# Optimization experiments

Measured on AMD Instinct MI355X. Metric: run time of the kernel, lower is better.

## Reference

```python
import jax, jax.numpy as jnp
import numpy as np

NUM_HEADS = 16
D_MODEL = 1024
D_QKV = 64


def _xavier(key, shape):
    # xavier normal over last two dims (fan_in = D_MODEL, fan_out = D_QKV)
    std = float(np.sqrt(2.0 / (shape[-2] + shape[-1])))
    return jax.random.normal(key, shape, dtype=jnp.float32) * std


def setup_inputs() -> dict:
    key = jax.random.key(0)
    ks = jax.random.split(key, 9)
    B, L = 4, 2048
    q = jax.random.normal(ks[0], (B, L, D_MODEL), dtype=jnp.float32)
    k = jax.random.normal(ks[1], (B, L, D_MODEL), dtype=jnp.float32)
    v = jax.random.normal(ks[2], (B, L, D_MODEL), dtype=jnp.float32)
    mask = jax.random.randint(ks[3], (B, L, L), 0, 2, dtype=jnp.int32)
    Wq = _xavier(ks[4], (NUM_HEADS, D_MODEL, D_QKV))
    Wk = _xavier(ks[5], (NUM_HEADS, D_MODEL, D_QKV))
    Wv = _xavier(ks[6], (NUM_HEADS, D_MODEL, D_QKV))
    lim = float(1.0 / np.sqrt(D_MODEL))
    Wo_w = jax.random.uniform(ks[7], (D_MODEL, D_MODEL), minval=-lim, maxval=lim, dtype=jnp.float32)
    Wo_b = jax.random.uniform(ks[8], (D_MODEL,), minval=-lim, maxval=lim, dtype=jnp.float32)
    return {"q": q, "k": k, "v": v, "mask": mask,
            "Wq": Wq, "Wk": Wk, "Wv": Wv, "Wo_w": Wo_w, "Wo_b": Wo_b}


def reference(q, k, v, mask, Wq, Wk, Wv, Wo_w, Wo_b):
    B, L, _ = q.shape
    query = jnp.einsum('blm,nmd->bnld', q, Wq)   # [B,H,L,Dq]
    key_ = jnp.einsum('blm,nmd->bnld', k, Wk)
    value = jnp.einsum('blm,nmd->bnld', v, Wv)
    scores = jnp.einsum('bnld,bnmd->bnlm', query, key_) / jnp.sqrt(
        jnp.asarray(D_QKV, dtype=query.dtype))          # [B,H,L,L]
    scores = jnp.where(mask[:, None, :, :] == 0, jnp.asarray(-1e9, scores.dtype), scores)
    attn = jax.nn.softmax(scores, axis=-1)
    out = jnp.einsum('bnlm,bnmd->bnld', attn, value)     # [B,H,L,Dq]
    out = out.transpose(0, 2, 1, 3).reshape(B, L, D_MODEL)
    return out @ Wo_w.T + Wo_b
```

## Files before the change

kernel.cpp:

```cpp
#include <hip/hip_runtime.h>
#include <stdint.h>

typedef __bf16 bf16;
typedef __bf16 bf16x8 __attribute__((ext_vector_type(8)));
typedef float  f32x4  __attribute__((ext_vector_type(4)));
typedef uint32_t u32;
typedef uint64_t u64;

#define SCALE_L2E 0.18033688011112042f

__device__ __forceinline__ void gld_lds16(const void* gsrc, void* ldst) {
  __builtin_amdgcn_global_load_lds(
      (const __attribute__((address_space(1))) void*)gsrc,
      (__attribute__((address_space(3))) void*)ldst, 16, 0, 0);
}


__global__ void cvt_f32_bf16(const float* __restrict__ in, bf16* __restrict__ out, int n8) {
  int stride = gridDim.x * blockDim.x;
  for (int i = blockIdx.x * blockDim.x + threadIdx.x; i < n8; i += stride) {
    const float4* p = (const float4*)(in + (size_t)i * 8);
    float4 a = p[0], b = p[1];
    bf16x8 v;
    v[0]=(bf16)a.x; v[1]=(bf16)a.y; v[2]=(bf16)a.z; v[3]=(bf16)a.w;
    v[4]=(bf16)b.x; v[5]=(bf16)b.y; v[6]=(bf16)b.z; v[7]=(bf16)b.w;
    *(bf16x8*)(out + (size_t)i * 8) = v;
  }
}

__global__ void pack_w(const float* __restrict__ Wq, const float* __restrict__ Wk,
                       const float* __restrict__ Wv, const float* __restrict__ Wo,
                       bf16* __restrict__ Wt) {
  int s = blockIdx.z;
  int tid = blockIdx.x * blockDim.x + threadIdx.x;
  int n = tid >> 7, kb = tid & 127;
  const float* W = (s == 0) ? Wq : (s == 1) ? Wk : (s == 2) ? Wv : Wo;
  bf16x8 v;
  if (s < 3) {
#pragma unroll
    for (int j = 0; j < 8; ++j)
      v[j] = (bf16)W[((n >> 6) << 16) + (kb * 8 + j) * 64 + (n & 63)];
  } else {
    const float4* p = (const float4*)&W[n * 1024 + kb * 8];
    float4 a = p[0], b = p[1];
    v[0]=(bf16)a.x; v[1]=(bf16)a.y; v[2]=(bf16)a.z; v[3]=(bf16)a.w;
    v[4]=(bf16)b.x; v[5]=(bf16)b.y; v[6]=(bf16)b.z; v[7]=(bf16)b.w;
  }
  *(bf16x8*)&Wt[(size_t)s * 1048576 + (size_t)n * 1024 + kb * 8] = v;
}

__global__ void pack_mask(const int* __restrict__ mask, u32* __restrict__ mbits, int total) {
  int stride = gridDim.x * blockDim.x;
  for (int idx = blockIdx.x * blockDim.x + threadIdx.x; idx < total; idx += stride) {
    int v = mask[idx];
    u64 bal = __ballot(v != 0);
    if ((threadIdx.x & 63) == 0)
      *(u64*)&mbits[idx >> 5] = bal;
  }
}

template<int EPI>
__global__ __launch_bounds__(256, 2)
void gemm_bt(const bf16* __restrict__ A, const bf16* __restrict__ Bt,
             void* __restrict__ Cout, const float* __restrict__ bias,
             size_t a_bstride, size_t b_bstride, float cscale) {
  const int gx = gridDim.x;
  int lin = blockIdx.y * gx + blockIdx.x;
  int nwg = gx * gridDim.y;
  int swz = (lin & 7) * (nwg >> 3) + (lin >> 3);
  int bx = swz % gx, by = swz / gx;
  const int bz = blockIdx.z;
  A  += a_bstride * bz;
  Bt += b_bstride * bz;
  const int row0 = by * 128, col0 = bx * 128;

  __shared__ bf16 sA[128 * 32];
  __shared__ bf16 sB[128 * 32];

  const int lane = threadIdx.x & 63, w = threadIdx.x >> 6;
  const int c = lane & 15, g = lane >> 4;
  const int wr = w >> 1, wc = w & 1;

  f32x4 acc[4][4] = {};

  const bf16* Ap = A + (size_t)row0 * 1024;
  const bf16* Bp = Bt + (size_t)col0 * 1024;

  for (int k0 = 0; k0 < 1024; k0 += 32) {
    __syncthreads();
#pragma unroll
    for (int i = 0; i < 2; ++i) {
      int u = (w * 2 + i) * 64 + lane;
      int r = u >> 2, part = u & 3;
      gld_lds16(Ap + (size_t)r * 1024 + k0 + part * 8, (char*)sA + (size_t)(w * 2 + i) * 1024);
      gld_lds16(Bp + (size_t)r * 1024 + k0 + part * 8, (char*)sB + (size_t)(w * 2 + i) * 1024);
    }
    __syncthreads();

    bf16x8 af[4], bfr[4];
#pragma unroll
    for (int m = 0; m < 4; ++m)
      af[m] = *(const bf16x8*)&sA[(wr * 64 + m * 16 + c) * 32 + g * 8];
#pragma unroll
    for (int n = 0; n < 4; ++n)
      bfr[n] = *(const bf16x8*)&sB[(wc * 64 + n * 16 + c) * 32 + g * 8];
#pragma unroll
    for (int m = 0; m < 4; ++m)
#pragma unroll
      for (int n = 0; n < 4; ++n)
        acc[m][n] = __builtin_amdgcn_mfma_f32_16x16x32_bf16(af[m], bfr[n], acc[m][n], 0, 0, 0);
  }

#pragma unroll
  for (int m = 0; m < 4; ++m) {
    int row_base = row0 + wr * 64 + m * 16 + g * 4;
#pragma unroll
    for (int n = 0; n < 4; ++n) {
      int col = col0 + wc * 64 + n * 16 + c;
#pragma unroll
      for (int r = 0; r < 4; ++r) {
        int row = row_base + r;
        float val = acc[m][n][r];
        if (EPI == 0) {
          int b = row >> 11, l = row & 2047, h = col >> 6, d = col & 63;
          ((bf16*)Cout)[(((size_t)(b * 16 + h) * 2048 + l) << 6) + d] = (bf16)(val * cscale);
        } else if (EPI == 1) {
          ((bf16*)Cout)[((size_t)(bz * 1024 + row)) * 2048 + col] = (bf16)val;
        } else {
          ((float*)Cout)[(size_t)row * 1024 + col] = val + bias[col];
        }
      }
    }
  }
}

__global__ __launch_bounds__(256, 3)
void attn_fwd(const bf16* __restrict__ Qp, const bf16* __restrict__ Kp,
              const bf16* __restrict__ Vt, const u32* __restrict__ mbits,
              bf16* __restrict__ X) {
  int lin = blockIdx.y * 16 + blockIdx.x;
  int swz = (lin & 7) * 128 + (lin >> 3);
  int qt = swz & 15, bh = swz >> 4;
  int b = bh >> 4, h = bh & 15;
  int q0 = qt * 128;

  const int tid = threadIdx.x;
  const int lane = tid & 63, w = tid >> 6;
  const int c = lane & 15, g = lane >> 4;

  __shared__ char smem[32768];
  char* sK = smem;
  char* sV = smem + 8192;
  char* sPw = smem + 16384 + w * 4096;

  const int c7 = c & 7;
  const int y0 = (g ^ c7) << 4;
  const int y1 = ((4 + g) ^ c7) << 4;
  const char* kaddr0 = sK + c * 128 + y0;
  const char* kaddr1 = sK + c * 128 + y1;
  const char* vaddr0 = sV + c * 128 + y0;
  const char* vaddr1 = sV + c * 128 + y1;
  const char* paddr0 = sPw + c * 128 + y0;
  const char* paddr1 = sPw + c * 128 + y1;
  char* pw[4];
#pragma unroll
  for (int nk = 0; nk < 4; ++nk)
    pw[nk] = sPw + c * 128 + ((g & 1) * 8) + (((nk * 2 + (g >> 1)) ^ c7) << 4);

  const int u1 = 256 + tid;
  const int r0 = tid >> 3, bb0 = tid & 7, r1 = u1 >> 3, bb1 = u1 & 7;
  char* dK0 = sK + r0 * 128 + ((bb0 ^ (r0 & 7)) << 4);
  char* dK1 = sK + r1 * 128 + ((bb1 ^ (r1 & 7)) << 4);
  char* dV0 = sV + r0 * 128 + ((bb0 ^ (r0 & 7)) << 4);
  char* dV1 = sV + r1 * 128 + ((bb1 ^ (r1 & 7)) << 4);
  const bf16* gK0 = Kp + (size_t)bh * 131072 + r0 * 64 + bb0 * 8;
  const bf16* gK1 = Kp + (size_t)bh * 131072 + r1 * 64 + bb1 * 8;
  const bf16* gV0 = Vt + ((size_t)(b * 1024 + h * 64 + r0)) * 2048 + bb0 * 8;
  const bf16* gV1 = Vt + ((size_t)(b * 1024 + h * 64 + r1)) * 2048 + bb1 * 8;

  const bf16* Qbase = Qp + ((size_t)bh * 2048) * 64;
  bf16x8 qf[2][2];
#pragma unroll
  for (int nq = 0; nq < 2; ++nq) {
    int qg = q0 + w * 32 + nq * 16 + c;
#pragma unroll
    for (int kk = 0; kk < 2; ++kk)
      qf[nq][kk] = *(const bf16x8*)&Qbase[(size_t)qg * 64 + kk * 32 + g * 8];
  }

  const u64* Mrow0 = (const u64*)(mbits + ((size_t)b * 2048 + (q0 + w * 32 + c)) * 64);
  const u64* Mrow1 = (const u64*)(mbits + ((size_t)b * 2048 + (q0 + w * 32 + 16 + c)) * 64);

  f32x4 oacc[4][2] = {};
  float lrun0 = 0.f, lrun1 = 0.f;

  uint4 kr0 = *(const uint4*)gK0, kr1 = *(const uint4*)gK1;
  uint4 vr0 = *(const uint4*)gV0, vr1 = *(const uint4*)gV1;
  u64 mw0 = Mrow0[0], mw1 = Mrow1[0];

  for (int t = 0; t < 32; ++t) {
    __syncthreads();
    *(uint4*)dK0 = kr0; *(uint4*)dK1 = kr1;
    *(uint4*)dV0 = vr0; *(uint4*)dV1 = vr1;
    __syncthreads();

    u64 mn0 = 0, mn1 = 0;
    if (t < 31) {
      kr0 = *(const uint4*)(gK0 + (size_t)(t + 1) * 4096);
      kr1 = *(const uint4*)(gK1 + (size_t)(t + 1) * 4096);
      vr0 = *(const uint4*)(gV0 + (size_t)(t + 1) * 64);
      vr1 = *(const uint4*)(gV1 + (size_t)(t + 1) * 64);
      mn0 = Mrow0[t + 1];
      mn1 = Mrow1[t + 1];
    }

    f32x4 st[4][2] = {};
#pragma unroll
    for (int nk = 0; nk < 4; ++nk) {
      bf16x8 kfa = *(const bf16x8*)(kaddr0 + nk * 2048);
      st[nk][0] = __builtin_amdgcn_mfma_f32_16x16x32_bf16(kfa, qf[0][0], st[nk][0], 0, 0, 0);
      st[nk][1] = __builtin_amdgcn_mfma_f32_16x16x32_bf16(kfa, qf[1][0], st[nk][1], 0, 0, 0);
      bf16x8 kfb = *(const bf16x8*)(kaddr1 + nk * 2048);
      st[nk][0] = __builtin_amdgcn_mfma_f32_16x16x32_bf16(kfb, qf[0][1], st[nk][0], 0, 0, 0);
      st[nk][1] = __builtin_amdgcn_mfma_f32_16x16x32_bf16(kfb, qf[1][1], st[nk][1], 0, 0, 0);
    }

#pragma unroll
    for (int nq = 0; nq < 2; ++nq) {
      u64 ms = (nq ? mw1 : mw0) >> (4 * g);
      u32 ma = (u32)ms;
      u32 mb = (u32)(ms >> 32);
      float ls = 0.f;
#pragma unroll
      for (int nk = 0; nk < 4; ++nk) {
        u32 msel = (nk < 2) ? ma : mb;
        const int bs = (nk & 1) * 16;
#pragma unroll
        for (int tt = 0; tt < 2; ++tt) {
          float e0 = __builtin_amdgcn_exp2f(st[nk][nq][tt * 2]);
          float e1 = __builtin_amdgcn_exp2f(st[nk][nq][tt * 2 + 1]);
          e0 = (msel & (1u << (bs + tt * 2)))     ? e0 : 0.f;
          e1 = (msel & (1u << (bs + tt * 2 + 1))) ? e1 : 0.f;
          ls += e0;
          ls += e1;
          union { bf16 h2[2]; u32 uu; } pk;
          pk.h2[0] = (bf16)e0; pk.h2[1] = (bf16)e1;
          *(u32*)(pw[nk] + nq * 2048 + tt * 4) = pk.uu;
        }
      }
      if (nq) lrun1 += ls; else lrun0 += ls;
    }

#pragma unroll
    for (int kk = 0; kk < 2; ++kk) {
      const char* pa = kk ? paddr1 : paddr0;
      const char* va = kk ? vaddr1 : vaddr0;
      bf16x8 pf0 = *(const bf16x8*)(pa);
      bf16x8 pf1 = *(const bf16x8*)(pa + 2048);
#pragma unroll
      for (int md = 0; md < 4; ++md) {
        bf16x8 vf = *(const bf16x8*)(va + md * 2048);
        oacc[md][0] = __builtin_amdgcn_mfma_f32_16x16x32_bf16(vf, pf0, oacc[md][0], 0, 0, 0);
        oacc[md][1] = __builtin_amdgcn_mfma_f32_16x16x32_bf16(vf, pf1, oacc[md][1], 0, 0, 0);
      }
    }

    mw0 = mn0; mw1 = mn1;
  }

  lrun0 += __shfl_xor(lrun0, 16); lrun0 += __shfl_xor(lrun0, 32);
  lrun1 += __shfl_xor(lrun1, 16); lrun1 += __shfl_xor(lrun1, 32);
  float inv0 = 1.f / lrun0;
  float inv1 = 1.f / lrun1;

  __syncthreads();
  char* Xl = smem;
#pragma unroll
  for (int nq = 0; nq < 2; ++nq) {
    float inv = nq ? inv1 : inv0;
    int ql = w * 32 + nq * 16 + c;
#pragma unroll
    for (int md = 0; md < 4; ++md)
#pragma unroll
      for (int r = 0; r < 4; ++r) {
        int d = md * 16 + g * 4 + r;
        int blk = d >> 3, off = d & 7;
        *(bf16*)(Xl + ql * 128 + ((blk ^ (ql & 7)) << 4) + off * 2) =
            (bf16)(oacc[md][nq][r] * inv);
      }
  }
  __syncthreads();
#pragma unroll
  for (int i = 0; i < 4; ++i) {
    int u = i * 256 + tid;
    int row = u >> 3, blk = u & 7;
    uint4 xv = *(const uint4*)(Xl + row * 128 + ((blk ^ (row & 7)) << 4));
    *(uint4*)&X[(size_t)(b * 2048 + q0 + row) * 1024 + h * 64 + blk * 8] = xv;
  }
}


extern "C" void kernel_launch(void* const* d_in, const int* in_sizes, int n_in,
                              void* d_out, int out_size, void* d_ws, size_t ws_size,
                              hipStream_t stream) {
  const float* q    = (const float*)d_in[0];
  const float* k    = (const float*)d_in[1];
  const float* v    = (const float*)d_in[2];
  const int*   mask = (const int*)d_in[3];
  const float* Wq   = (const float*)d_in[4];
  const float* Wk   = (const float*)d_in[5];
  const float* Wv   = (const float*)d_in[6];
  const float* Wo   = (const float*)d_in[7];
  const float* Wb   = (const float*)d_in[8];

  char* ws = (char*)d_ws;
  bf16* qb = (bf16*)(ws + 0);
  bf16* kb = (bf16*)(ws + 16777216);
  bf16* vb = (bf16*)(ws + 33554432);
  bf16* Wt = (bf16*)(ws + 50331648);
  bf16* Qp = (bf16*)(ws + 58720256);
  bf16* Kp = (bf16*)(ws + 75497472);
  bf16* Vt = (bf16*)(ws + 92274688);
  bf16* Xb = (bf16*)(ws + 109051904);
  u32*  mb = (u32*) (ws + 125829120);

  cvt_f32_bf16<<<1024, 256, 0, stream>>>(q, qb, 1048576);
  cvt_f32_bf16<<<1024, 256, 0, stream>>>(k, kb, 1048576);
  cvt_f32_bf16<<<1024, 256, 0, stream>>>(v, vb, 1048576);
  pack_w<<<dim3(512, 1, 4), 256, 0, stream>>>(Wq, Wk, Wv, Wo, Wt);
  pack_mask<<<2048, 256, 0, stream>>>(mask, mb, 16777216);

  gemm_bt<0><<<dim3(8, 64, 1), 256, 0, stream>>>(qb, Wt,            Qp, nullptr, 0, 0, SCALE_L2E);
  gemm_bt<0><<<dim3(8, 64, 1), 256, 0, stream>>>(kb, Wt + 1048576,  Kp, nullptr, 0, 0, 1.0f);
  gemm_bt<1><<<dim3(16, 8, 4), 256, 0, stream>>>(Wt + 2097152, vb,  Vt, nullptr, 0, 2097152, 1.0f);

  attn_fwd<<<dim3(16, 64, 1), 256, 0, stream>>>(Qp, Kp, Vt, mb, Xb);

  gemm_bt<2><<<dim3(8, 64, 1), 256, 0, stream>>>(Xb, Wt + 3145728, (float*)d_out, Wb, 0, 0, 1.0f);
}
```

Baseline: 289.2 us.

## Double-buffer LDS in GEMM and attention, merge conversion and Q/K projection launches

The projection GEMM now double-buffers its LDS tiles. The next k-slice's global_load_lds is issued before computing on the current slice, so only one barrier per iteration is needed. The attention kernel double-buffers its K/V LDS tiles (48KB of LDS) and writes the prefetched registers into the alternate buffer after the PV MFMAs, which removes one barrier per tile. The three f32-to-bf16 conversions are merged into one launch, and the Q and K projections are merged into one GEMM launch with a per-block output and scale selection. The intent is less barrier stall and launch overhead, at the cost of more LDS per block, which could reduce occupancy.

```diff
diff --git a/kernel.cpp b/kernel.cpp
--- a/kernel.cpp
+++ b/kernel.cpp
@@ -16,15 +16,18 @@
 }
 
 
-__global__ void cvt_f32_bf16(const float* __restrict__ in, bf16* __restrict__ out, int n8) {
+__global__ void cvt3(const float* __restrict__ q, const float* __restrict__ k,
+                     const float* __restrict__ v, bf16* __restrict__ out) {
+  const float* in = (blockIdx.z == 0) ? q : (blockIdx.z == 1) ? k : v;
+  bf16* o = out + (size_t)blockIdx.z * 8388608;
   int stride = gridDim.x * blockDim.x;
-  for (int i = blockIdx.x * blockDim.x + threadIdx.x; i < n8; i += stride) {
+  for (int i = blockIdx.x * blockDim.x + threadIdx.x; i < 1048576; i += stride) {
     const float4* p = (const float4*)(in + (size_t)i * 8);
     float4 a = p[0], b = p[1];
-    bf16x8 v;
-    v[0]=(bf16)a.x; v[1]=(bf16)a.y; v[2]=(bf16)a.z; v[3]=(bf16)a.w;
-    v[4]=(bf16)b.x; v[5]=(bf16)b.y; v[6]=(bf16)b.z; v[7]=(bf16)b.w;
-    *(bf16x8*)(out + (size_t)i * 8) = v;
+    bf16x8 vv;
+    vv[0]=(bf16)a.x; vv[1]=(bf16)a.y; vv[2]=(bf16)a.z; vv[3]=(bf16)a.w;
+    vv[4]=(bf16)b.x; vv[5]=(bf16)b.y; vv[6]=(bf16)b.z; vv[7]=(bf16)b.w;
+    *(bf16x8*)(o + (size_t)i * 8) = vv;
   }
 }
 
@@ -62,7 +65,8 @@
 template<int EPI>
 __global__ __launch_bounds__(256, 2)
 void gemm_bt(const bf16* __restrict__ A, const bf16* __restrict__ Bt,
-             void* __restrict__ Cout, const float* __restrict__ bias,
+             void* __restrict__ Cout, void* __restrict__ Cout2,
+             const float* __restrict__ bias,
              size_t a_bstride, size_t b_bstride, float cscale) {
   const int gx = gridDim.x;
   int lin = blockIdx.y * gx + blockIdx.x;
@@ -73,37 +77,50 @@
   A  += a_bstride * bz;
   Bt += b_bstride * bz;
   const int row0 = by * 128, col0 = bx * 128;
-
-  __shared__ bf16 sA[128 * 32];
-  __shared__ bf16 sB[128 * 32];
+  bool isK = false;
+  if (EPI == 0 && row0 >= 8192) { isK = true; Bt += 1048576; }
+
+  __shared__ bf16 sA[2][4096];
+  __shared__ bf16 sB[2][4096];
 
   const int lane = threadIdx.x & 63, w = threadIdx.x >> 6;
   const int c = lane & 15, g = lane >> 4;
   const int wr = w >> 1, wc = w & 1;
 
-  f32x4 acc[4][4] = {};
-
+  const int u0 = w * 128 + lane;
+  const int rs0 = u0 >> 2, ps0 = u0 & 3;
+  const int rs1 = (u0 + 64) >> 2, ps1 = (u0 + 64) & 3;
   const bf16* Ap = A + (size_t)row0 * 1024;
   const bf16* Bp = Bt + (size_t)col0 * 1024;
+  const bf16* As0 = Ap + (size_t)rs0 * 1024 + ps0 * 8;
+  const bf16* As1 = Ap + (size_t)rs1 * 1024 + ps1 * 8;
+  const bf16* Bs0 = Bp + (size_t)rs0 * 1024 + ps0 * 8;
+  const bf16* Bs1 = Bp + (size_t)rs1 * 1024 + ps1 * 8;
+
+  f32x4 acc[4][4] = {};
+
+  gld_lds16(As0, (char*)&sA[0][0] + (w * 2) * 1024);
+  gld_lds16(As1, (char*)&sA[0][0] + (w * 2 + 1) * 1024);
+  gld_lds16(Bs0, (char*)&sB[0][0] + (w * 2) * 1024);
+  gld_lds16(Bs1, (char*)&sB[0][0] + (w * 2 + 1) * 1024);
 
   for (int k0 = 0; k0 < 1024; k0 += 32) {
     __syncthreads();
-#pragma unroll
-    for (int i = 0; i < 2; ++i) {
-      int u = (w * 2 + i) * 64 + lane;
-      int r = u >> 2, part = u & 3;
-      gld_lds16(Ap + (size_t)r * 1024 + k0 + part * 8, (char*)sA + (size_t)(w * 2 + i) * 1024);
-      gld_lds16(Bp + (size_t)r * 1024 + k0 + part * 8, (char*)sB + (size_t)(w * 2 + i) * 1024);
-    }
-    __syncthreads();
+    int cb = (k0 >> 5) & 1, nb = cb ^ 1;
+    if (k0 < 992) {
+      gld_lds16(As0 + k0 + 32, (char*)&sA[nb][0] + (w * 2) * 1024);
+      gld_lds16(As1 + k0 + 32, (char*)&sA[nb][0] + (w * 2 + 1) * 1024);
+      gld_lds16(Bs0 + k0 + 32, (char*)&sB[nb][0] + (w * 2) * 1024);
+      gld_lds16(Bs1 + k0 + 32, (char*)&sB[nb][0] + (w * 2 + 1) * 1024);
+    }
 
     bf16x8 af[4], bfr[4];
 #pragma unroll
     for (int m = 0; m < 4; ++m)
-      af[m] = *(const bf16x8*)&sA[(wr * 64 + m * 16 + c) * 32 + g * 8];
+      af[m] = *(const bf16x8*)&sA[cb][(wr * 64 + m * 16 + c) * 32 + g * 8];
 #pragma unroll
     for (int n = 0; n < 4; ++n)
-      bfr[n] = *(const bf16x8*)&sB[(wc * 64 + n * 16 + c) * 32 + g * 8];
+      bfr[n] = *(const bf16x8*)&sB[cb][(wc * 64 + n * 16 + c) * 32 + g * 8];
 #pragma unroll
     for (int m = 0; m < 4; ++m)
 #pragma unroll
@@ -111,6 +128,7 @@
         acc[m][n] = __builtin_amdgcn_mfma_f32_16x16x32_bf16(af[m], bfr[n], acc[m][n], 0, 0, 0);
   }
 
+  float csc = (EPI == 0 && isK) ? 1.0f : cscale;
 #pragma unroll
   for (int m = 0; m < 4; ++m) {
     int row_base = row0 + wr * 64 + m * 16 + g * 4;
@@ -122,8 +140,10 @@
         int row = row_base + r;
         float val = acc[m][n][r];
         if (EPI == 0) {
-          int b = row >> 11, l = row & 2047, h = col >> 6, d = col & 63;
-          ((bf16*)Cout)[(((size_t)(b * 16 + h) * 2048 + l) << 6) + d] = (bf16)(val * cscale);
+          int rl = row & 8191;
+          int b = rl >> 11, l = rl & 2047, h = col >> 6, d = col & 63;
+          bf16* dst = isK ? (bf16*)Cout2 : (bf16*)Cout;
+          dst[(((size_t)(b * 16 + h) * 2048 + l) << 6) + d] = (bf16)(val * csc);
         } else if (EPI == 1) {
           ((bf16*)Cout)[((size_t)(bz * 1024 + row)) * 2048 + col] = (bf16)val;
         } else {
@@ -148,18 +168,17 @@
   const int lane = tid & 63, w = tid >> 6;
   const int c = lane & 15, g = lane >> 4;
 
-  __shared__ char smem[32768];
-  char* sK = smem;
-  char* sV = smem + 8192;
-  char* sPw = smem + 16384 + w * 4096;
+  __shared__ char smem[49152];
+  char* sKV = smem;
+  char* sPw = smem + 32768 + w * 4096;
 
   const int c7 = c & 7;
   const int y0 = (g ^ c7) << 4;
   const int y1 = ((4 + g) ^ c7) << 4;
-  const char* kaddr0 = sK + c * 128 + y0;
-  const char* kaddr1 = sK + c * 128 + y1;
-  const char* vaddr0 = sV + c * 128 + y0;
-  const char* vaddr1 = sV + c * 128 + y1;
+  const int ko0 = c * 128 + y0;
+  const int ko1 = c * 128 + y1;
+  const int vo0 = 8192 + c * 128 + y0;
+  const int vo1 = 8192 + c * 128 + y1;
   const char* paddr0 = sPw + c * 128 + y0;
   const char* paddr1 = sPw + c * 128 + y1;
   char* pw[4];
@@ -167,12 +186,12 @@
   for (int nk = 0; nk < 4; ++nk)
     pw[nk] = sPw + c * 128 + ((g & 1) * 8) + (((nk * 2 + (g >> 1)) ^ c7) << 4);
 
-  const int u1 = 256 + tid;
-  const int r0 = tid >> 3, bb0 = tid & 7, r1 = u1 >> 3, bb1 = u1 & 7;
-  char* dK0 = sK + r0 * 128 + ((bb0 ^ (r0 & 7)) << 4);
-  char* dK1 = sK + r1 * 128 + ((bb1 ^ (r1 & 7)) << 4);
-  char* dV0 = sV + r0 * 128 + ((bb0 ^ (r0 & 7)) << 4);
-  char* dV1 = sV + r1 * 128 + ((bb1 ^ (r1 & 7)) << 4);
+  const int r0 = tid >> 3, bb0 = tid & 7;
+  const int r1 = (256 + tid) >> 3, bb1 = tid & 7;
+  const int dK0 = r0 * 128 + ((bb0 ^ (r0 & 7)) << 4);
+  const int dK1 = r1 * 128 + ((bb1 ^ (r1 & 7)) << 4);
+  const int dV0 = 8192 + dK0;
+  const int dV1 = 8192 + dK1;
   const bf16* gK0 = Kp + (size_t)bh * 131072 + r0 * 64 + bb0 * 8;
   const bf16* gK1 = Kp + (size_t)bh * 131072 + r1 * 64 + bb1 * 8;
   const bf16* gV0 = Vt + ((size_t)(b * 1024 + h * 64 + r0)) * 2048 + bb0 * 8;
@@ -194,16 +213,19 @@
   f32x4 oacc[4][2] = {};
   float lrun0 = 0.f, lrun1 = 0.f;
 
-  uint4 kr0 = *(const uint4*)gK0, kr1 = *(const uint4*)gK1;
-  uint4 vr0 = *(const uint4*)gV0, vr1 = *(const uint4*)gV1;
+  {
+    uint4 kr0 = *(const uint4*)gK0, kr1 = *(const uint4*)gK1;
+    uint4 vr0 = *(const uint4*)gV0, vr1 = *(const uint4*)gV1;
+    *(uint4*)(sKV + dK0) = kr0; *(uint4*)(sKV + dK1) = kr1;
+    *(uint4*)(sKV + dV0) = vr0; *(uint4*)(sKV + dV1) = vr1;
+  }
   u64 mw0 = Mrow0[0], mw1 = Mrow1[0];
 
   for (int t = 0; t < 32; ++t) {
     __syncthreads();
-    *(uint4*)dK0 = kr0; *(uint4*)dK1 = kr1;
-    *(uint4*)dV0 = vr0; *(uint4*)dV1 = vr1;
-    __syncthreads();
-
+    const char* kbuf = sKV + ((t & 1) << 14);
+
+    uint4 kr0, kr1, vr0, vr1;
     u64 mn0 = 0, mn1 = 0;
     if (t < 31) {
       kr0 = *(const uint4*)(gK0 + (size_t)(t + 1) * 4096);
@@ -217,10 +239,10 @@
     f32x4 st[4][2] = {};
 #pragma unroll
     for (int nk = 0; nk < 4; ++nk) {
-      bf16x8 kfa = *(const bf16x8*)(kaddr0 + nk * 2048);
+      bf16x8 kfa = *(const bf16x8*)(kbuf + ko0 + nk * 2048);
       st[nk][0] = __builtin_amdgcn_mfma_f32_16x16x32_bf16(kfa, qf[0][0], st[nk][0], 0, 0, 0);
       st[nk][1] = __builtin_amdgcn_mfma_f32_16x16x32_bf16(kfa, qf[1][0], st[nk][1], 0, 0, 0);
-      bf16x8 kfb = *(const bf16x8*)(kaddr1 + nk * 2048);
+      bf16x8 kfb = *(const bf16x8*)(kbuf + ko1 + nk * 2048);
       st[nk][0] = __builtin_amdgcn_mfma_f32_16x16x32_bf16(kfb, qf[0][1], st[nk][0], 0, 0, 0);
       st[nk][1] = __builtin_amdgcn_mfma_f32_16x16x32_bf16(kfb, qf[1][1], st[nk][1], 0, 0, 0);
     }
@@ -254,17 +276,22 @@
 #pragma unroll
     for (int kk = 0; kk < 2; ++kk) {
       const char* pa = kk ? paddr1 : paddr0;
-      const char* va = kk ? vaddr1 : vaddr0;
+      const int vo = kk ? vo1 : vo0;
       bf16x8 pf0 = *(const bf16x8*)(pa);
       bf16x8 pf1 = *(const bf16x8*)(pa + 2048);
 #pragma unroll
       for (int md = 0; md < 4; ++md) {
-        bf16x8 vf = *(const bf16x8*)(va + md * 2048);
+        bf16x8 vf = *(const bf16x8*)(kbuf + vo + md * 2048);
         oacc[md][0] = __builtin_amdgcn_mfma_f32_16x16x32_bf16(vf, pf0, oacc[md][0], 0, 0, 0);
         oacc[md][1] = __builtin_amdgcn_mfma_f32_16x16x32_bf16(vf, pf1, oacc[md][1], 0, 0, 0);
       }
     }
 
+    if (t < 31) {
+      char* nbuf = sKV + (((t + 1) & 1) << 14);
+      *(uint4*)(nbuf + dK0) = kr0; *(uint4*)(nbuf + dK1) = kr1;
+      *(uint4*)(nbuf + dV0) = vr0; *(uint4*)(nbuf + dV1) = vr1;
+    }
     mw0 = mn0; mw1 = mn1;
   }
 
@@ -324,17 +351,14 @@
   bf16* Xb = (bf16*)(ws + 109051904);
   u32*  mb = (u32*) (ws + 125829120);
 
-  cvt_f32_bf16<<<1024, 256, 0, stream>>>(q, qb, 1048576);
-  cvt_f32_bf16<<<1024, 256, 0, stream>>>(k, kb, 1048576);
-  cvt_f32_bf16<<<1024, 256, 0, stream>>>(v, vb, 1048576);
+  cvt3<<<dim3(512, 1, 3), 256, 0, stream>>>(q, k, v, qb);
   pack_w<<<dim3(512, 1, 4), 256, 0, stream>>>(Wq, Wk, Wv, Wo, Wt);
   pack_mask<<<2048, 256, 0, stream>>>(mask, mb, 16777216);
 
-  gemm_bt<0><<<dim3(8, 64, 1), 256, 0, stream>>>(qb, Wt,            Qp, nullptr, 0, 0, SCALE_L2E);
-  gemm_bt<0><<<dim3(8, 64, 1), 256, 0, stream>>>(kb, Wt + 1048576,  Kp, nullptr, 0, 0, 1.0f);
-  gemm_bt<1><<<dim3(16, 8, 4), 256, 0, stream>>>(Wt + 2097152, vb,  Vt, nullptr, 0, 2097152, 1.0f);
+  gemm_bt<0><<<dim3(8, 128, 1), 256, 0, stream>>>(qb, Wt, Qp, Kp, nullptr, 0, 0, SCALE_L2E);
+  gemm_bt<1><<<dim3(16, 8, 4), 256, 0, stream>>>(Wt + 2097152, vb, Vt, nullptr, nullptr, 0, 2097152, 1.0f);
 
   attn_fwd<<<dim3(16, 64, 1), 256, 0, stream>>>(Qp, Kp, Vt, mb, Xb);
 
-  gemm_bt<2><<<dim3(8, 64, 1), 256, 0, stream>>>(Xb, Wt + 3145728, (float*)d_out, Wb, 0, 0, 1.0f);
-}
+  gemm_bt<2><<<dim3(8, 64, 1), 256, 0, stream>>>(Xb, Wt + 3145728, (float*)d_out, nullptr, Wb, 0, 0, 1.0f);
+}
```

Result: faster. 263.9 us (-8.7%).
